# Kernel optimization log

Measured on AMD Instinct MI355X. Metric: run time of the kernel, lower is better.

The kernel has to match this reference:

```python
import jax, jax.numpy as jnp
import numpy as np

VOCAB = 128000
HID = 128
OUT = 5
N_TREES = 16
N_LEAVES = 64


def _build_trees():
    # Post-order (children before parent) node arrays for N_TREES balanced
    # binary trees; indices are global across the whole batch of trees.
    is_leaf, left, right = [], [], []
    def rec(nl):
        if nl == 1:
            i = len(is_leaf)
            is_leaf.append(True); left.append(i); right.append(i)
            return i
        l = rec(nl // 2)
        r = rec(nl - nl // 2)
        i = len(is_leaf)
        is_leaf.append(False); left.append(l); right.append(r)
        return i
    for _ in range(N_TREES):
        rec(N_LEAVES)
    return (np.array(is_leaf), np.array(left, np.int64), np.array(right, np.int64))


def setup_inputs() -> dict:
    key = jax.random.key(0)
    ks = jax.random.split(key, 8)
    il, l, r = _build_trees()
    n = il.shape[0]  # 2032
    word_idx = jax.random.randint(ks[0], (n,), 0, VOCAB)
    s = 0.05  # scale randn params so tanh does not fully saturate
    return {
        "embed": jax.random.normal(ks[1], (VOCAB, HID), jnp.float32) * s,
        "V": jax.random.normal(ks[2], (HID, 2 * HID, 2 * HID), jnp.float32) * s,
        "W": jax.random.normal(ks[3], (2 * HID, HID), jnp.float32) * s,
        "b": jax.random.normal(ks[4], (1, HID), jnp.float32) * s,
        "Wout_w": jax.random.normal(ks[5], (HID, OUT), jnp.float32) * s,
        "Wout_b": jax.random.normal(ks[6], (OUT,), jnp.float32) * s,
        "is_leaf": jnp.asarray(il),
        "word_idx": word_idx,
        "left_idx": jnp.asarray(l),
        "right_idx": jnp.asarray(r),
    }


def _forward(embed, V, W, b, Wout_w, Wout_b, is_leaf, word_idx, left_idx, right_idx):
    n = is_leaf.shape[0]
    h = W.shape[1]

    def step(Hs, xs):
        i, lf, w, l, r = xs
        c = jnp.concatenate([Hs[l], Hs[r]])              # [2h] concat of children
        xVx = jnp.einsum('k,hkl,l->h', c, V, c)          # bilinear V term, one scalar per slice
        internal = jnp.tanh(xVx + c @ W + b[0])          # [h]
        cur = jnp.where(lf, embed[w], internal)          # leaf -> embedding lookup
        return Hs.at[i].set(cur), None

    H0 = jnp.zeros((n, h), dtype=embed.dtype)
    Hs, _ = jax.lax.scan(
        step, H0,
        (jnp.arange(n), is_leaf, word_idx, left_idx, right_idx))
    # all-node output (root_only=False): log_softmax(W_out(h))
    return jax.nn.log_softmax(Hs @ Wout_w + Wout_b, axis=1)


def reference(embed, V, W, b, Wout_w, Wout_b, is_leaf, word_idx, left_idx, right_idx):
    return _forward(embed, V, W, b, Wout_w, Wout_b,
                    is_leaf, word_idx, left_idx, right_idx)
```

## Files before the change

kernel.cpp:

```cpp
#include <hip/hip_runtime.h>

#define HID 128
#define NODES 2032
#define NPT 127
#define NW 1024

typedef _Float16 f16x8 __attribute__((ext_vector_type(8)));
typedef _Float16 f16x4 __attribute__((ext_vector_type(4)));
typedef float f32x4 __attribute__((ext_vector_type(4)));

__device__ __forceinline__ int tree_idx(int p, int sst) {
  return (p + 1) * sst + p - __popc(p) - 1;
}
__device__ __forceinline__ int cswz(int row, int colbyte) {
  return row * 512 + (colbyte ^ ((row & 31) << 4));
}

__device__ __forceinline__ unsigned int cload(const void* p) {
  return __hip_atomic_load((const unsigned int*)p, __ATOMIC_RELAXED, __HIP_MEMORY_SCOPE_AGENT);
}
__device__ __forceinline__ void cstore(void* p, unsigned int v) {
  __hip_atomic_store((unsigned int*)p, v, __ATOMIC_RELAXED, __HIP_MEMORY_SCOPE_AGENT);
}
__device__ __forceinline__ float cloadf(const void* p) {
  union { unsigned int u; float f; } c; c.u = cload(p); return c.f;
}
__device__ __forceinline__ void cstoref(void* p, float f) {
  union { float f; unsigned int u; } c; c.f = f; cstore(p, c.u);
}

__device__ __forceinline__ void gbar(int* sb, int ph) {
  asm volatile("s_waitcnt vmcnt(0)" ::: "memory");
  __syncthreads();
  if (threadIdx.x == 0) {
    int* base = sb + ph * 1024;
    const int grp = blockIdx.x & 15;
    int v = __hip_atomic_fetch_add(base + grp * 32, 1, __ATOMIC_RELAXED, __HIP_MEMORY_SCOPE_AGENT);
    if (v == 15) {
      int r = __hip_atomic_fetch_add(base + 768, 1, __ATOMIC_RELAXED, __HIP_MEMORY_SCOPE_AGENT);
      if (r == 15)
        __hip_atomic_store(base + 800, 1, __ATOMIC_RELAXED, __HIP_MEMORY_SCOPE_AGENT);
    }
    while (!__hip_atomic_load(base + 800, __ATOMIC_RELAXED, __HIP_MEMORY_SCOPE_AGENT))
      __builtin_amdgcn_s_sleep(4);
  }
  __syncthreads();
}

__global__ __launch_bounds__(256, 1) void rntn_kernel(
    const float* __restrict__ V, const float* __restrict__ W, const float* __restrict__ bb,
    const float* __restrict__ embed, const int* __restrict__ word_idx,
    const float* __restrict__ Wout, const float* __restrict__ Wb,
    _Float16* __restrict__ H16A, _Float16* __restrict__ H16B,
    float* __restrict__ Hgt, float* __restrict__ out, int* __restrict__ syncb)
{
  __shared__ _Float16 Alds[256 * 256];
  __shared__ _Float16 Ct[32 * 256];
  __shared__ float red[4][32];

  const int bid = blockIdx.x;
  const int h = bid >> 1, part = bid & 1;
  const int tid = threadIdx.x, lane = tid & 63, w = tid >> 6;
  const int lo16 = lane & 15, q = lane >> 4;
  const int nidx = tid & 31, oct = tid >> 5;
  char* ab = (char*)Alds;
  char* cb = (char*)Ct;

  {
    const float* src = V + (size_t)h * 65536 + (size_t)tid * 256;
#pragma unroll
    for (int u2 = 0; u2 < 32; ++u2) {
      const float4 a = ((const float4*)src)[u2 * 2];
      const float4 b2 = ((const float4*)src)[u2 * 2 + 1];
      f16x8 v;
      v[0] = (_Float16)a.x;  v[1] = (_Float16)a.y;
      v[2] = (_Float16)a.z;  v[3] = (_Float16)a.w;
      v[4] = (_Float16)b2.x; v[5] = (_Float16)b2.y;
      v[6] = (_Float16)b2.z; v[7] = (_Float16)b2.w;
      *(f16x8*)(ab + cswz(tid, u2 * 16)) = v;
    }
  }
  f32x4 wk[4];
#pragma unroll
  for (int rf = 0; rf < 4; ++rf) {
    const int kb = w * 64 + rf * 16 + q * 4;
#pragma unroll
    for (int i = 0; i < 4; ++i)
      wk[rf][i] = W[(size_t)(kb + i) * HID + h];
  }
  const float bh = bb[h];
  __syncthreads();

  for (int lv = 0; lv < 6; ++lv) {
    const int m = 512 >> lv;
    const int lognpt = 5 - lv;
    const int sst = (1 << (lv + 2)) - 1;
    _Float16* Hp = (lv & 1) ? H16A : H16B;
    _Float16* Hn = (lv & 1) ? H16B : H16A;
    const int nodes_blk = m >> 1;
    const int n_start = part * nodes_blk;
    const int ntiles = (nodes_blk + 31) >> 5;

    unsigned int u[16];
    if (lv > 0) {
      const int nn0 = nodes_blk > 32 ? 32 : nodes_blk;
      if (nidx < nn0) {
#pragma unroll
        for (int half = 0; half < 2; ++half)
#pragma unroll
          for (int j = 0; j < 8; ++j)
            u[half * 8 + j] = cload(Hp + (size_t)(half * 64 + oct * 8 + j) * NW
                                       + 2 * (n_start + nidx));
      }
    }

    for (int t = 0; t < ntiles; ++t) {
      const int nb = n_start + t * 32;
      int nn = nodes_blk - t * 32; if (nn > 32) nn = 32;
      const int ncf = (nn + 15) >> 4;

      __syncthreads();
      if (lv == 0) {
        const int r4 = tid >> 2, seg = tid & 3;
        if (r4 < 2 * nn) {
          const int nodeL = r4 >> 1, child = r4 & 1;
          const int lp = 2 * (nb + nodeL) + child;
          const int tt = lp >> 6, pp = lp & 63;
          const int g = tt * NPT + 2 * pp - __popc(pp);
          const int wi = word_idx[g];
          const float* src = embed + (size_t)wi * HID + seg * 32;
#pragma unroll
          for (int u2 = 0; u2 < 4; ++u2) {
            const float4 a = ((const float4*)src)[u2 * 2];
            const float4 b2 = ((const float4*)src)[u2 * 2 + 1];
            f16x8 v;
            v[0] = (_Float16)a.x;  v[1] = (_Float16)a.y;
            v[2] = (_Float16)a.z;  v[3] = (_Float16)a.w;
            v[4] = (_Float16)b2.x; v[5] = (_Float16)b2.y;
            v[6] = (_Float16)b2.z; v[7] = (_Float16)b2.w;
            *(f16x8*)(cb + cswz(nodeL, child * 256 + seg * 64 + u2 * 16)) = v;
          }
        }
      } else {
        if (nidx < nn) {
          union { f16x8 v; unsigned short s[8]; } a0, a1;
#pragma unroll
          for (int half = 0; half < 2; ++half) {
#pragma unroll
            for (int j = 0; j < 8; ++j) {
              a0.s[j] = (unsigned short)(u[half * 8 + j] & 0xffffu);
              a1.s[j] = (unsigned short)(u[half * 8 + j] >> 16);
            }
            *(f16x8*)(cb + cswz(nidx, half * 128 + oct * 16)) = a0.v;
            *(f16x8*)(cb + cswz(nidx, 256 + half * 128 + oct * 16)) = a1.v;
          }
        }
      }
      __syncthreads();

      if (lv > 0 && t + 1 < ntiles) {
        int nnn = nodes_blk - (t + 1) * 32; if (nnn > 32) nnn = 32;
        if (nidx < nnn) {
#pragma unroll
          for (int half = 0; half < 2; ++half)
#pragma unroll
            for (int j = 0; j < 8; ++j)
              u[half * 8 + j] = cload(Hp + (size_t)(half * 64 + oct * 8 + j) * NW
                                         + 2 * (nb + 32 + nidx));
        }
      }

      f32x4 acc[4][2];
#pragma unroll
      for (int rf = 0; rf < 4; ++rf)
#pragma unroll
        for (int cf = 0; cf < 2; ++cf) { f32x4 z = {0.f, 0.f, 0.f, 0.f}; acc[rf][cf] = z; }

#pragma unroll
      for (int lc = 0; lc < 8; ++lc) {
        f16x8 Af[4];
#pragma unroll
        for (int rf = 0; rf < 4; ++rf)
          Af[rf] = *(const f16x8*)(ab + cswz(w * 64 + rf * 16 + lo16, lc * 64 + q * 16));
#pragma unroll
        for (int cf = 0; cf < 2; ++cf) {
          if (cf < ncf) {
            const int nl = cf * 16 + lo16;
            const f16x8 Bf = *(const f16x8*)(cb + cswz(nl, lc * 64 + q * 16));
#pragma unroll
            for (int rf = 0; rf < 4; ++rf)
              acc[rf][cf] = __builtin_amdgcn_mfma_f32_16x16x32_f16(Af[rf], Bf, acc[rf][cf], 0, 0, 0);
          }
        }
      }

      float pt[2];
#pragma unroll
      for (int cf = 0; cf < 2; ++cf) {
        pt[cf] = 0.f;
        if (cf < ncf) {
          const int nl = cf * 16 + lo16;
          float s = 0.f;
#pragma unroll
          for (int rf = 0; rf < 4; ++rf) {
            const int kb = w * 64 + rf * 16 + q * 4;
            const f16x4 cv = *(const f16x4*)(cb + cswz(nl, kb * 2));
            s += (float)cv[0] * (acc[rf][cf][0] + wk[rf][0])
               + (float)cv[1] * (acc[rf][cf][1] + wk[rf][1])
               + (float)cv[2] * (acc[rf][cf][2] + wk[rf][2])
               + (float)cv[3] * (acc[rf][cf][3] + wk[rf][3]);
          }
          pt[cf] = s;
        }
      }
#pragma unroll
      for (int cf = 0; cf < 2; ++cf) {
        pt[cf] += __shfl_xor(pt[cf], 16);
        pt[cf] += __shfl_xor(pt[cf], 32);
      }
      if (q == 0) {
#pragma unroll
        for (int cf = 0; cf < 2; ++cf)
          if (cf < ncf) red[w][cf * 16 + lo16] = pt[cf];
      }
      __syncthreads();

      if (tid < (nn >> 1)) {
        const float x0 = red[0][2 * tid] + red[1][2 * tid] + red[2][2 * tid] + red[3][2 * tid] + bh;
        const float x1 = red[0][2 * tid + 1] + red[1][2 * tid + 1] + red[2][2 * tid + 1] + red[3][2 * tid + 1] + bh;
        const float t0 = tanhf(x0), t1 = tanhf(x1);
        union { _Float16 f; unsigned short s; } c0, c1;
        c0.f = (_Float16)t0; c1.f = (_Float16)t1;
        const int n0 = nb + 2 * tid;
        cstore(Hn + (size_t)h * NW + n0, (unsigned)c0.s | ((unsigned)c1.s << 16));
        const int mask = (1 << lognpt) - 1;
        const int g0 = ((n0) >> lognpt) * NPT + tree_idx(n0 & mask, sst);
        const int g1 = ((n0 + 1) >> lognpt) * NPT + tree_idx((n0 + 1) & mask, sst);
        cstoref(Hgt + (size_t)h * 2048 + g0, t0);
        cstoref(Hgt + (size_t)h * 2048 + g1, t1);
      }
      if (lv == 0 && tid < 2 * nn) {
        const int nodeL = tid >> 1, child = tid & 1;
        const int lp = 2 * (nb + nodeL) + child;
        const int tt = lp >> 6, pp = lp & 63;
        const int g = tt * NPT + 2 * pp - __popc(pp);
        const _Float16 hv = *(const _Float16*)(cb + cswz(nodeL, child * 256 + 2 * h));
        cstoref(Hgt + (size_t)h * 2048 + g, (float)hv);
      }
    }
    gbar(syncb, lv);
  }

  if (bid < 127) {
    const int node = bid * 16 + (tid >> 4);
    const int hs = tid & 15;
    float l0 = 0.f, l1 = 0.f, l2 = 0.f, l3 = 0.f, l4 = 0.f;
#pragma unroll
    for (int j = 0; j < 8; ++j) {
      const int hh = hs + j * 16;
      const float x = cloadf(Hgt + (size_t)hh * 2048 + node);
      const float* wr = Wout + (size_t)hh * 5;
      l0 += x * wr[0]; l1 += x * wr[1]; l2 += x * wr[2];
      l3 += x * wr[3]; l4 += x * wr[4];
    }
#pragma unroll
    for (int d = 1; d < 16; d <<= 1) {
      l0 += __shfl_xor(l0, d); l1 += __shfl_xor(l1, d); l2 += __shfl_xor(l2, d);
      l3 += __shfl_xor(l3, d); l4 += __shfl_xor(l4, d);
    }
    if (hs == 0) {
      l0 += Wb[0]; l1 += Wb[1]; l2 += Wb[2]; l3 += Wb[3]; l4 += Wb[4];
      const float mm = fmaxf(fmaxf(fmaxf(l0, l1), fmaxf(l2, l3)), l4);
      const float ss = expf(l0 - mm) + expf(l1 - mm) + expf(l2 - mm)
                     + expf(l3 - mm) + expf(l4 - mm);
      const float lse = mm + logf(ss);
      float* o = out + (size_t)node * 5;
      o[0] = l0 - lse; o[1] = l1 - lse; o[2] = l2 - lse; o[3] = l3 - lse; o[4] = l4 - lse;
    }
  }
}

extern "C" void kernel_launch(void* const* d_in, const int* in_sizes, int n_in,
                              void* d_out, int out_size, void* d_ws, size_t ws_size,
                              hipStream_t stream) {
  const float* embed = (const float*)d_in[0];
  const float* V     = (const float*)d_in[1];
  const float* W     = (const float*)d_in[2];
  const float* b     = (const float*)d_in[3];
  const float* Wout  = (const float*)d_in[4];
  const float* Woutb = (const float*)d_in[5];
  const int* word_idx = (const int*)d_in[7];
  float* out = (float*)d_out;

  char* wsb = (char*)d_ws;
  _Float16* H16A = (_Float16*)wsb;
  _Float16* H16B = (_Float16*)(wsb + 262144);
  float*    Hgt  = (float*)(wsb + 524288);
  int*     syncb = (int*)(wsb + 1572864);

  hipMemsetAsync(syncb, 0, 32768, stream);
  rntn_kernel<<<256, 256, 0, stream>>>(V, W, b, embed, word_idx, Wout, Woutb,
                                       H16A, H16B, Hgt, out, syncb);
}
```

Before: 83.64 us.

## Double block size to 512 threads and prefetch leaf embeddings into registers

Each block now runs 8 waves instead of 4, so every wave handles 32 rows of the V slice rather than 64. This halves per-wave MFMA work and the accumulator registers, and spreads the V staging and child-state loads across more threads. Leaf embeddings for the first tile are loaded into registers before V staging, and later tiles are prefetched during compute, so the level-0 gather latency is hidden. The cost is a cross-wave reduction over 8 partial sums and more threads taking part in each barrier.

Result: faster. 76.41 us (-8.6%).

```diff
diff --git a/kernel.cpp b/kernel.cpp
--- a/kernel.cpp
+++ b/kernel.cpp
@@ -47,7 +47,7 @@
   __syncthreads();
 }
 
-__global__ __launch_bounds__(256, 1) void rntn_kernel(
+__global__ __launch_bounds__(512, 1) void rntn_kernel(
     const float* __restrict__ V, const float* __restrict__ W, const float* __restrict__ bb,
     const float* __restrict__ embed, const int* __restrict__ word_idx,
     const float* __restrict__ Wout, const float* __restrict__ Wb,
@@ -56,20 +56,34 @@
 {
   __shared__ _Float16 Alds[256 * 256];
   __shared__ _Float16 Ct[32 * 256];
-  __shared__ float red[4][32];
+  __shared__ float red[8][32];
 
   const int bid = blockIdx.x;
   const int h = bid >> 1, part = bid & 1;
   const int tid = threadIdx.x, lane = tid & 63, w = tid >> 6;
   const int lo16 = lane & 15, q = lane >> 4;
   const int nidx = tid & 31, oct = tid >> 5;
+  const int r8 = tid >> 3, seg = tid & 7;
   char* ab = (char*)Alds;
   char* cb = (char*)Ct;
 
+  float4 ef0, ef1, ef2, ef3;
   {
-    const float* src = V + (size_t)h * 65536 + (size_t)tid * 256;
-#pragma unroll
-    for (int u2 = 0; u2 < 32; ++u2) {
+    const int nodeL = r8 >> 1, child = r8 & 1;
+    const int lp = 2 * (part * 256 + nodeL) + child;
+    const int tt = lp >> 6, pp = lp & 63;
+    const int g = tt * NPT + 2 * pp - __popc(pp);
+    const int wi = word_idx[g];
+    const float* src = embed + (size_t)wi * HID + seg * 16;
+    ef0 = ((const float4*)src)[0]; ef1 = ((const float4*)src)[1];
+    ef2 = ((const float4*)src)[2]; ef3 = ((const float4*)src)[3];
+  }
+
+  {
+    const int arow = tid >> 1, ahalf = tid & 1;
+    const float* src = V + (size_t)h * 65536 + (size_t)arow * 256 + ahalf * 128;
+#pragma unroll
+    for (int u2 = 0; u2 < 16; ++u2) {
       const float4 a = ((const float4*)src)[u2 * 2];
       const float4 b2 = ((const float4*)src)[u2 * 2 + 1];
       f16x8 v;
@@ -77,13 +91,13 @@
       v[2] = (_Float16)a.z;  v[3] = (_Float16)a.w;
       v[4] = (_Float16)b2.x; v[5] = (_Float16)b2.y;
       v[6] = (_Float16)b2.z; v[7] = (_Float16)b2.w;
-      *(f16x8*)(ab + cswz(tid, u2 * 16)) = v;
-    }
-  }
-  f32x4 wk[4];
-#pragma unroll
-  for (int rf = 0; rf < 4; ++rf) {
-    const int kb = w * 64 + rf * 16 + q * 4;
+      *(f16x8*)(ab + cswz(arow, ahalf * 256 + u2 * 16)) = v;
+    }
+  }
+  f32x4 wk[2];
+#pragma unroll
+  for (int rf = 0; rf < 2; ++rf) {
+    const int kb = w * 32 + rf * 16 + q * 4;
 #pragma unroll
     for (int i = 0; i < 4; ++i)
       wk[rf][i] = W[(size_t)(kb + i) * HID + h];
@@ -101,16 +115,13 @@
     const int n_start = part * nodes_blk;
     const int ntiles = (nodes_blk + 31) >> 5;
 
-    unsigned int u[16];
+    unsigned int u[8];
     if (lv > 0) {
       const int nn0 = nodes_blk > 32 ? 32 : nodes_blk;
       if (nidx < nn0) {
 #pragma unroll
-        for (int half = 0; half < 2; ++half)
-#pragma unroll
-          for (int j = 0; j < 8; ++j)
-            u[half * 8 + j] = cload(Hp + (size_t)(half * 64 + oct * 8 + j) * NW
-                                       + 2 * (n_start + nidx));
+        for (int j = 0; j < 8; ++j)
+          u[j] = cload(Hp + (size_t)(oct * 8 + j) * NW + 2 * (n_start + nidx));
       }
     }
 
@@ -121,74 +132,71 @@
 
       __syncthreads();
       if (lv == 0) {
-        const int r4 = tid >> 2, seg = tid & 3;
-        if (r4 < 2 * nn) {
-          const int nodeL = r4 >> 1, child = r4 & 1;
-          const int lp = 2 * (nb + nodeL) + child;
+        f16x8 v0, v1;
+        v0[0] = (_Float16)ef0.x; v0[1] = (_Float16)ef0.y;
+        v0[2] = (_Float16)ef0.z; v0[3] = (_Float16)ef0.w;
+        v0[4] = (_Float16)ef1.x; v0[5] = (_Float16)ef1.y;
+        v0[6] = (_Float16)ef1.z; v0[7] = (_Float16)ef1.w;
+        v1[0] = (_Float16)ef2.x; v1[1] = (_Float16)ef2.y;
+        v1[2] = (_Float16)ef2.z; v1[3] = (_Float16)ef2.w;
+        v1[4] = (_Float16)ef3.x; v1[5] = (_Float16)ef3.y;
+        v1[6] = (_Float16)ef3.z; v1[7] = (_Float16)ef3.w;
+        const int nodeL = r8 >> 1, child = r8 & 1;
+        *(f16x8*)(cb + cswz(nodeL, child * 256 + seg * 32)) = v0;
+        *(f16x8*)(cb + cswz(nodeL, child * 256 + seg * 32 + 16)) = v1;
+      } else {
+        if (nidx < nn) {
+          union { f16x8 v; unsigned short s[8]; } a0, a1;
+#pragma unroll
+          for (int j = 0; j < 8; ++j) {
+            a0.s[j] = (unsigned short)(u[j] & 0xffffu);
+            a1.s[j] = (unsigned short)(u[j] >> 16);
+          }
+          *(f16x8*)(cb + cswz(nidx, oct * 16)) = a0.v;
+          *(f16x8*)(cb + cswz(nidx, 256 + oct * 16)) = a1.v;
+        }
+      }
+      __syncthreads();
+
+      if (t + 1 < ntiles) {
+        if (lv == 0) {
+          const int nodeL = r8 >> 1, child = r8 & 1;
+          const int lp = 2 * (nb + 32 + nodeL) + child;
           const int tt = lp >> 6, pp = lp & 63;
           const int g = tt * NPT + 2 * pp - __popc(pp);
           const int wi = word_idx[g];
-          const float* src = embed + (size_t)wi * HID + seg * 32;
-#pragma unroll
-          for (int u2 = 0; u2 < 4; ++u2) {
-            const float4 a = ((const float4*)src)[u2 * 2];
-            const float4 b2 = ((const float4*)src)[u2 * 2 + 1];
-            f16x8 v;
-            v[0] = (_Float16)a.x;  v[1] = (_Float16)a.y;
-            v[2] = (_Float16)a.z;  v[3] = (_Float16)a.w;
-            v[4] = (_Float16)b2.x; v[5] = (_Float16)b2.y;
-            v[6] = (_Float16)b2.z; v[7] = (_Float16)b2.w;
-            *(f16x8*)(cb + cswz(nodeL, child * 256 + seg * 64 + u2 * 16)) = v;
+          const float* src = embed + (size_t)wi * HID + seg * 16;
+          ef0 = ((const float4*)src)[0]; ef1 = ((const float4*)src)[1];
+          ef2 = ((const float4*)src)[2]; ef3 = ((const float4*)src)[3];
+        } else {
+          int nnn = nodes_blk - (t + 1) * 32; if (nnn > 32) nnn = 32;
+          if (nidx < nnn) {
+#pragma unroll
+            for (int j = 0; j < 8; ++j)
+              u[j] = cload(Hp + (size_t)(oct * 8 + j) * NW + 2 * (nb + 32 + nidx));
           }
         }
-      } else {
-        if (nidx < nn) {
-          union { f16x8 v; unsigned short s[8]; } a0, a1;
-#pragma unroll
-          for (int half = 0; half < 2; ++half) {
-#pragma unroll
-            for (int j = 0; j < 8; ++j) {
-              a0.s[j] = (unsigned short)(u[half * 8 + j] & 0xffffu);
-              a1.s[j] = (unsigned short)(u[half * 8 + j] >> 16);
-            }
-            *(f16x8*)(cb + cswz(nidx, half * 128 + oct * 16)) = a0.v;
-            *(f16x8*)(cb + cswz(nidx, 256 + half * 128 + oct * 16)) = a1.v;
-          }
-        }
-      }
-      __syncthreads();
-
-      if (lv > 0 && t + 1 < ntiles) {
-        int nnn = nodes_blk - (t + 1) * 32; if (nnn > 32) nnn = 32;
-        if (nidx < nnn) {
-#pragma unroll
-          for (int half = 0; half < 2; ++half)
-#pragma unroll
-            for (int j = 0; j < 8; ++j)
-              u[half * 8 + j] = cload(Hp + (size_t)(half * 64 + oct * 8 + j) * NW
-                                         + 2 * (nb + 32 + nidx));
-        }
-      }
-
-      f32x4 acc[4][2];
-#pragma unroll
-      for (int rf = 0; rf < 4; ++rf)
+      }
+
+      f32x4 acc[2][2];
+#pragma unroll
+      for (int rf = 0; rf < 2; ++rf)
 #pragma unroll
         for (int cf = 0; cf < 2; ++cf) { f32x4 z = {0.f, 0.f, 0.f, 0.f}; acc[rf][cf] = z; }
 
 #pragma unroll
       for (int lc = 0; lc < 8; ++lc) {
-        f16x8 Af[4];
-#pragma unroll
-        for (int rf = 0; rf < 4; ++rf)
-          Af[rf] = *(const f16x8*)(ab + cswz(w * 64 + rf * 16 + lo16, lc * 64 + q * 16));
+        f16x8 Af[2];
+#pragma unroll
+        for (int rf = 0; rf < 2; ++rf)
+          Af[rf] = *(const f16x8*)(ab + cswz(w * 32 + rf * 16 + lo16, lc * 64 + q * 16));
 #pragma unroll
         for (int cf = 0; cf < 2; ++cf) {
           if (cf < ncf) {
             const int nl = cf * 16 + lo16;
             const f16x8 Bf = *(const f16x8*)(cb + cswz(nl, lc * 64 + q * 16));
 #pragma unroll
-            for (int rf = 0; rf < 4; ++rf)
+            for (int rf = 0; rf < 2; ++rf)
               acc[rf][cf] = __builtin_amdgcn_mfma_f32_16x16x32_f16(Af[rf], Bf, acc[rf][cf], 0, 0, 0);
           }
         }
@@ -202,8 +210,8 @@
           const int nl = cf * 16 + lo16;
           float s = 0.f;
 #pragma unroll
-          for (int rf = 0; rf < 4; ++rf) {
-            const int kb = w * 64 + rf * 16 + q * 4;
+          for (int rf = 0; rf < 2; ++rf) {
+            const int kb = w * 32 + rf * 16 + q * 4;
             const f16x4 cv = *(const f16x4*)(cb + cswz(nl, kb * 2));
             s += (float)cv[0] * (acc[rf][cf][0] + wk[rf][0])
                + (float)cv[1] * (acc[rf][cf][1] + wk[rf][1])
@@ -226,8 +234,12 @@
       __syncthreads();
 
       if (tid < (nn >> 1)) {
-        const float x0 = red[0][2 * tid] + red[1][2 * tid] + red[2][2 * tid] + red[3][2 * tid] + bh;
-        const float x1 = red[0][2 * tid + 1] + red[1][2 * tid + 1] + red[2][2 * tid + 1] + red[3][2 * tid + 1] + bh;
+        float x0 = bh, x1 = bh;
+#pragma unroll
+        for (int ww = 0; ww < 8; ++ww) {
+          x0 += red[ww][2 * tid];
+          x1 += red[ww][2 * tid + 1];
+        }
         const float t0 = tanhf(x0), t1 = tanhf(x1);
         union { _Float16 f; unsigned short s; } c0, c1;
         c0.f = (_Float16)t0; c1.f = (_Float16)t1;
@@ -251,7 +263,7 @@
     gbar(syncb, lv);
   }
 
-  if (bid < 127) {
+  if (bid < 127 && tid < 256) {
     const int node = bid * 16 + (tid >> 4);
     const int hs = tid & 15;
     float l0 = 0.f, l1 = 0.f, l2 = 0.f, l3 = 0.f, l4 = 0.f;
@@ -299,6 +311,6 @@
   int*     syncb = (int*)(wsb + 1572864);
 
   hipMemsetAsync(syncb, 0, 32768, stream);
-  rntn_kernel<<<256, 256, 0, stream>>>(V, W, b, embed, word_idx, Wout, Woutb,
+  rntn_kernel<<<256, 512, 0, stream>>>(V, W, b, embed, word_idx, Wout, Woutb,
                                        H16A, H16B, Hgt, out, syncb);
 }
```
